# Performance work log

Measured on AMD Instinct MI355X. Metric: run time of the kernel, lower is better.

The kernel has to match this reference:

```python
import jax, jax.numpy as jnp
import numpy as np

N = 50000      # nodes
E = 1_600_000  # edges (avg degree 32)
IN = 256
HID = 64
H = 4          # heads
OUT = 128
NEG = 0.2      # LeakyReLU negative slope


def setup_inputs() -> dict:
    key = jax.random.key(0)
    ks = jax.random.split(key, 16)
    def p(i, shape):
        return jax.random.normal(ks[i], shape, jnp.float32) * 0.05
    x = jax.random.normal(ks[0], (N, IN), jnp.float32)
    edge_index = jax.random.randint(ks[1], (2, E), 0, N, dtype=jnp.int64)
    return dict(
        x=x, edge_index=edge_index,
        W0=p(2, (IN, H * HID)), as0=p(3, (H, HID)), ad0=p(4, (H, HID)), b0=p(5, (H * HID,)),
        W1=p(6, (H * HID, H * HID)), as1=p(7, (H, HID)), ad1=p(8, (H, HID)), b1=p(9, (H * HID,)),
        W2=p(10, (H * HID, OUT)), as2=p(11, (1, OUT)), ad2=p(12, (1, OUT)), b2=p(13, (OUT,)),
        Wl=p(14, (H * HID, OUT)), bl=p(15, (OUT,)),
    )


def gat_conv(x, src, dst, W, a_s, a_d, b, heads, ch):
    # Linear projection -> per-head features [N, H, C]
    h = (x @ W).reshape(-1, heads, ch)
    # Per-node attention logits [N, H]
    al_s = jnp.einsum('nhc,hc->nh', h, a_s)
    al_d = jnp.einsum('nhc,hc->nh', h, a_d)
    # Per-edge logits: gather + LeakyReLU  [E2, H]
    e = jax.nn.leaky_relu(al_s[src] + al_d[dst], NEG)
    # Segment softmax over destination neighborhoods (stable)
    m = jax.ops.segment_max(e, dst, num_segments=N)
    e = jnp.exp(e - m[dst])
    s = jax.ops.segment_sum(e, dst, num_segments=N)
    a = e / s[dst]
    # Weighted scatter-add aggregation [N, H, C]
    out = jax.ops.segment_sum(a[:, :, None] * h[src], dst, num_segments=N)
    return out.reshape(N, heads * ch) + b


def reference(x, edge_index, W0, as0, ad0, b0, W1, as1, ad1, b1, W2, as2, ad2, b2, Wl, bl):
    # add self-loops (PyG GATConv default)
    loop = jnp.arange(N, dtype=edge_index.dtype)
    src = jnp.concatenate([edge_index[0], loop])
    dst = jnp.concatenate([edge_index[1], loop])
    # layer 0: in -> hid*heads (no residual at layer 0)
    h0 = gat_conv(x, src, dst, W0, as0, ad0, b0, H, HID)
    # layer 1: hid*heads -> hid*heads, residual
    h1 = gat_conv(h0, src, dst, W1, as1, ad1, b1, H, HID) + h0
    # layer 2 (last): hid*heads -> out with 1 head, residual via last_linear
    h2 = gat_conv(h1, src, dst, W2, as2, ad2, b2, 1, OUT) + (h1 @ Wl + bl)
    return h2
```

## Files before the change

kernel.cpp:

```cpp
#include <hip/hip_runtime.h>
#include <hip/hip_bf16.h>

#define N_NODES 50000
#define N_EDGES 1600000
#define E2 (N_EDGES + N_NODES)
#define NB 782
#define BCAP 3072
#define CHUNK 8192
#define NBLK_E 202

typedef __attribute__((ext_vector_type(8))) short bf16x8;
typedef __attribute__((ext_vector_type(4))) float f32x4;

static __device__ __forceinline__ float lrelu(float x) { return x > 0.f ? x : 0.2f * x; }

static __device__ __forceinline__ float b2f(ushort u) {
    union { unsigned int u; float f; } v;
    v.u = ((unsigned int)u) << 16;
    return v.f;
}
static __device__ __forceinline__ float hi2f(unsigned int u) {
    union { unsigned int u; float f; } v;
    v.u = u & 0xffff0000u;
    return v.f;
}
static __device__ __forceinline__ float lo2f(unsigned int u) {
    union { unsigned int u; float f; } v;
    v.u = u << 16;
    return v.f;
}
static __device__ __forceinline__ ushort f2b(float f) {
    union { float f; unsigned int u; } v;
    v.f = f;
    unsigned int r = v.u + 0x7FFFu + ((v.u >> 16) & 1u);
    return (ushort)(r >> 16);
}


__global__ __launch_bounds__(256) void k_bhist(const int* __restrict__ edst, int* __restrict__ hist) {
    __shared__ int cnt[NB];
    int t = threadIdx.x;
    for (int i = t; i < NB; i += 256) cnt[i] = 0;
    __syncthreads();
    int e0 = blockIdx.x * CHUNK;
    int eend = min(e0 + CHUNK, E2);
    for (int e = e0 + t; e < eend; e += 256) {
        int d = (e < N_EDGES) ? edst[e] : (e - N_EDGES);
        atomicAdd(&cnt[d >> 6], 1);
    }
    __syncthreads();
    for (int i = t; i < NB; i += 256) hist[blockIdx.x * NB + i] = cnt[i];
}

__global__ __launch_bounds__(1024) void k_colscan(const int* __restrict__ hist,
                                                  int* __restrict__ start, int* __restrict__ btotal) {
    int b = threadIdx.x;
    if (b >= NB) return;
    int run = 0;
#pragma unroll 4
    for (int blk = 0; blk < NBLK_E; ++blk) {
        int v = hist[blk * NB + b];
        start[blk * NB + b] = run;
        run += v;
    }
    btotal[b] = run;
}

__global__ __launch_bounds__(256) void k_bscan(const int* __restrict__ btotal, int* __restrict__ bbase,
                                               int* __restrict__ rowptr) {
    __shared__ int s[256];
    int t = threadIdx.x;
    int v[4];
    int sum = 0;
#pragma unroll
    for (int k = 0; k < 4; ++k) {
        int i = t * 4 + k;
        v[k] = (i < NB) ? btotal[i] : 0;
        sum += v[k];
    }
    s[t] = sum;
    __syncthreads();
    for (int off = 1; off < 256; off <<= 1) {
        int add = (t >= off) ? s[t - off] : 0;
        __syncthreads();
        s[t] += add;
        __syncthreads();
    }
    int base = s[t] - sum;
#pragma unroll
    for (int k = 0; k < 4; ++k) {
        int i = t * 4 + k;
        if (i < NB) bbase[i] = base;
        base += v[k];
    }
    if (t == 0) rowptr[N_NODES] = E2;
}

__global__ __launch_bounds__(256) void k_bscatter(const int* __restrict__ esrc, const int* __restrict__ edst,
                                                  const int* __restrict__ start, const int* __restrict__ bbase,
                                                  unsigned int* __restrict__ bbuf) {
    __shared__ int cnt[NB];
    __shared__ int cur[NB];
    __shared__ int gofs[NB];
    __shared__ int s_scan[256];
    __shared__ unsigned int s_e[CHUNK];
    int t = threadIdx.x;
    for (int i = t; i < NB; i += 256) cnt[i] = 0;
    __syncthreads();
    int e0 = blockIdx.x * CHUNK;
    int eend = min(e0 + CHUNK, E2);
    for (int e = e0 + t; e < eend; e += 256) {
        int d = (e < N_EDGES) ? edst[e] : (e - N_EDGES);
        atomicAdd(&cnt[d >> 6], 1);
    }
    __syncthreads();
    int v[4];
    int sum = 0;
#pragma unroll
    for (int k = 0; k < 4; ++k) {
        int i = t * 4 + k;
        v[k] = (i < NB) ? cnt[i] : 0;
        sum += v[k];
    }
    s_scan[t] = sum;
    __syncthreads();
    for (int off = 1; off < 256; off <<= 1) {
        int add = (t >= off) ? s_scan[t - off] : 0;
        __syncthreads();
        s_scan[t] += add;
        __syncthreads();
    }
    int run = s_scan[t] - sum;
#pragma unroll
    for (int k = 0; k < 4; ++k) {
        int i = t * 4 + k;
        if (i < NB) {
            cur[i] = run;
            gofs[i] = bbase[i] + start[blockIdx.x * NB + i] - run;
        }
        run += v[k];
    }
    __syncthreads();
    for (int e = e0 + t; e < eend; e += 256) {
        int s, d;
        if (e < N_EDGES) { s = esrc[e]; d = edst[e]; } else { s = d = e - N_EDGES; }
        int b = d >> 6;
        int pos = atomicAdd(&cur[b], 1);
        s_e[pos] = (unsigned int)s | ((unsigned int)(d & 63) << 16) | ((unsigned int)b << 22);
    }
    __syncthreads();
    int cntall = eend - e0;
    for (int i = t; i < cntall; i += 256) {
        unsigned int p = s_e[i];
        int b = p >> 22;
        bbuf[gofs[b] + i] = p & 0x3FFFFFu;
    }
}

__global__ __launch_bounds__(256) void k_build(const int* __restrict__ btotal, const int* __restrict__ bbase,
                                               const unsigned int* __restrict__ bbuf,
                                               int* __restrict__ rowptr, int* __restrict__ col) {
    const int b = blockIdx.x;
    const int t = threadIdx.x;
    const int cnt = btotal[b];
    const int base = bbase[b];
    const int node0 = b << 6;

    __shared__ unsigned int s_e[BCAP];
    __shared__ int s_deg[64];
    __shared__ int s_cur[64];

    if (t < 64) s_deg[t] = 0;
    __syncthreads();
    for (int i = t; i < cnt; i += 256) {
        unsigned int p = bbuf[(size_t)base + i];
        s_e[i] = p;
        atomicAdd(&s_deg[(p >> 16) & 63], 1);
    }
    __syncthreads();
    if (t < 64) {
        int d = s_deg[t];
        int incl = d;
#pragma unroll
        for (int off = 1; off < 64; off <<= 1) {
            int o = __shfl_up(incl, off);
            if (t >= off) incl += o;
        }
        int startl = incl - d;
        s_cur[t] = startl;
        int node = node0 + t;
        if (node < N_NODES) rowptr[node] = base + startl;
    }
    __syncthreads();
    for (int i = t; i < cnt; i += 256) {
        unsigned int p = s_e[i];
        int pos = atomicAdd(&s_cur[(p >> 16) & 63], 1);
        col[base + pos] = (int)(p & 0xFFFFu);
    }
}


__global__ void k_quant(const float* __restrict__ x, ushort* __restrict__ xb, int n4) {
    int i = blockIdx.x * 256 + threadIdx.x;
    if (i >= n4) return;
    float4 v = ((const float4*)x)[i];
    ushort4 o;
    o.x = f2b(v.x); o.y = f2b(v.y); o.z = f2b(v.z); o.w = f2b(v.w);
    ((ushort4*)xb)[i] = o;
}

__global__ void k_wt(const float* __restrict__ W, ushort* __restrict__ Wt) {
    int i = blockIdx.x * 256 + threadIdx.x;
    int k = i >> 8, n = i & 255;
    Wt[n * 256 + k] = f2b(W[i]);
}

__global__ void k_wtc(const float* __restrict__ W2, const float* __restrict__ Wl, ushort* __restrict__ Wt) {
    int i = blockIdx.x * 256 + threadIdx.x;
    int k = i >> 8, n = i & 255;
    float v = (n < 128) ? W2[k * 128 + n] : Wl[k * 128 + (n - 128)];
    Wt[n * 256 + k] = f2b(v);
}


template <bool FUSE>
__global__ __launch_bounds__(256) void k_mfma(const ushort* __restrict__ A, const ushort* __restrict__ Bt,
                                              ushort* __restrict__ Cb, int M,
                                              const float* __restrict__ a_s, const float* __restrict__ a_d,
                                              float* __restrict__ als, float* __restrict__ ald) {
    const int t = threadIdx.x;
    const int w = t >> 6, l = t & 63;
    const int lr = l & 15, lk = l >> 4;
    const int m0 = blockIdx.x * 32;
    const int n0 = w * 64;
    f32x4 acc[2][4] = {};

    int r0 = m0 + lr;      if (r0 >= M) r0 = M - 1;
    int r1 = m0 + 16 + lr; if (r1 >= M) r1 = M - 1;
    const ushort* a0p = A + (size_t)r0 * 256 + lk * 8;
    const ushort* a1p = A + (size_t)r1 * 256 + lk * 8;
    const ushort* bp  = Bt + (size_t)(n0 + lr) * 256 + lk * 8;

#pragma unroll
    for (int k0 = 0; k0 < 256; k0 += 32) {
        bf16x8 a0 = *(const bf16x8*)(a0p + k0);
        bf16x8 a1 = *(const bf16x8*)(a1p + k0);
#pragma unroll
        for (int n = 0; n < 4; ++n) {
            bf16x8 b = *(const bf16x8*)(bp + n * 16 * 256 + k0);
            acc[0][n] = __builtin_amdgcn_mfma_f32_16x16x32_bf16(a0, b, acc[0][n], 0, 0, 0);
            acc[1][n] = __builtin_amdgcn_mfma_f32_16x16x32_bf16(a1, b, acc[1][n], 0, 0, 0);
        }
    }

#pragma unroll
    for (int m = 0; m < 2; ++m) {
#pragma unroll
        for (int r = 0; r < 4; ++r) {
            int row = m0 + m * 16 + lk * 4 + r;
            if (row >= M) continue;
#pragma unroll
            for (int n = 0; n < 4; ++n) {
                Cb[(size_t)row * 256 + n0 + n * 16 + lr] = f2b(acc[m][n][r]);
            }
        }
    }

    if constexpr (FUSE) {
        float asc[4], adc[4];
#pragma unroll
        for (int n = 0; n < 4; ++n) {
            int c = n0 + n * 16 + lr;
            asc[n] = a_s[c];
            adc[n] = a_d[c];
        }
#pragma unroll
        for (int m = 0; m < 2; ++m) {
#pragma unroll
            for (int r = 0; r < 4; ++r) {
                float pa = 0.f, pd = 0.f;
#pragma unroll
                for (int n = 0; n < 4; ++n) {
                    pa += acc[m][n][r] * asc[n];
                    pd += acc[m][n][r] * adc[n];
                }
#pragma unroll
                for (int off = 1; off < 16; off <<= 1) {
                    pa += __shfl_xor(pa, off);
                    pd += __shfl_xor(pd, off);
                }
                if (lr == 0) {
                    int row = m0 + m * 16 + lk * 4 + r;
                    if (row < M) {
                        als[row * 4 + w] = pa;
                        ald[row * 4 + w] = pd;
                    }
                }
            }
        }
    }
}


template <int HEADS, int CHAN>
__global__ __launch_bounds__(256) void k_al(const ushort* __restrict__ Pb,
                                            const float* __restrict__ a_s, const float* __restrict__ a_d,
                                            float* __restrict__ als, float* __restrict__ ald) {
    int n = blockIdx.x * 4 + (threadIdx.x >> 6);
    if (n >= N_NODES) return;
    int l = threadIdx.x & 63;
    const ushort* row = Pb + (size_t)n * 256;
#pragma unroll
    for (int h = 0; h < HEADS; ++h) {
        float ps = 0.f, pd = 0.f;
#pragma unroll
        for (int c = l; c < CHAN; c += 64) {
            float v = b2f(row[h * CHAN + c]);
            ps += v * a_s[h * CHAN + c];
            pd += v * a_d[h * CHAN + c];
        }
#pragma unroll
        for (int off = 32; off > 0; off >>= 1) {
            ps += __shfl_xor(ps, off);
            pd += __shfl_xor(pd, off);
        }
        if (l == 0) { als[n * HEADS + h] = ps; ald[n * HEADS + h] = pd; }
    }
}


template <int HEADS>
__device__ __forceinline__ void load_als(const float* __restrict__ als, int src, float* v) {
    if constexpr (HEADS == 4) {
        float4 a = *(const float4*)(als + (size_t)src * 4);
        v[0] = a.x; v[1] = a.y; v[2] = a.z; v[3] = a.w;
    } else {
        v[0] = als[src];
    }
}


template <int HEADS, int CHAN, bool RESB, bool LIN, bool WRITEF, bool WRITEB>
__global__ __launch_bounds__(256) void k_aggw(
    const ushort* __restrict__ Pb,
    const float* __restrict__ als, const float* __restrict__ ald,
    const int* __restrict__ rowptr, const int* __restrict__ col,
    const float* __restrict__ bias, const float* __restrict__ bias2,
    const ushort* __restrict__ residb, float* __restrict__ out, ushort* __restrict__ outb) {
    constexpr int BLK = HEADS * CHAN;
    constexpr int CPL = BLK / 64;
    const int t = threadIdx.x;
    const int w = t >> 6, l = t & 63;
    const int n = blockIdx.x * 4 + w;
    const int rs = rowptr[n];
    const int deg = rowptr[n + 1] - rs;

    __shared__ int s_src[4][64];
    __shared__ float s_w[4][64 * HEADS];

    float aldn[HEADS];
    load_als<HEADS>(ald, n, aldn);

    float acc[CPL];
#pragma unroll
    for (int c = 0; c < CPL; ++c) acc[c] = 0.f;
    float sw[HEADS];
#pragma unroll
    for (int h = 0; h < HEADS; ++h) sw[h] = 0.f;

    const int hsel = l >> 4;

    for (int base = 0; base < deg; base += 64) {
        int j = base + l;
        if (j < deg) {
            int src = col[rs + j];
            s_src[w][l] = src;
            float av[HEADS];
            load_als<HEADS>(als, src, av);
#pragma unroll
            for (int h = 0; h < HEADS; ++h) {
                float wv = __expf(lrelu(av[h] + aldn[h]));
                s_w[w][l * HEADS + h] = wv;
                sw[h] += wv;
            }
        }
        int cnt = min(64, deg - base);
        int jj = 0;
        for (; jj + 2 <= cnt; jj += 2) {
            int s0 = __builtin_amdgcn_readfirstlane(s_src[w][jj]);
            int s1 = __builtin_amdgcn_readfirstlane(s_src[w][jj + 1]);
            if constexpr (CPL == 4) {
                float w0 = s_w[w][jj * HEADS + hsel];
                float w1 = s_w[w][(jj + 1) * HEADS + hsel];
                uint2 v0 = *(const uint2*)(Pb + (size_t)s0 * 256 + l * 4);
                uint2 v1 = *(const uint2*)(Pb + (size_t)s1 * 256 + l * 4);
                acc[0] += w0 * lo2f(v0.x); acc[1] += w0 * hi2f(v0.x);
                acc[2] += w0 * lo2f(v0.y); acc[3] += w0 * hi2f(v0.y);
                acc[0] += w1 * lo2f(v1.x); acc[1] += w1 * hi2f(v1.x);
                acc[2] += w1 * lo2f(v1.y); acc[3] += w1 * hi2f(v1.y);
            } else {
                float w0 = s_w[w][jj];
                float w1 = s_w[w][jj + 1];
                unsigned int v0 = *(const unsigned int*)(Pb + (size_t)s0 * 256 + l * 2);
                unsigned int v1 = *(const unsigned int*)(Pb + (size_t)s1 * 256 + l * 2);
                acc[0] += w0 * lo2f(v0); acc[1] += w0 * hi2f(v0);
                acc[0] += w1 * lo2f(v1); acc[1] += w1 * hi2f(v1);
            }
        }
        if (jj < cnt) {
            int s0 = __builtin_amdgcn_readfirstlane(s_src[w][jj]);
            if constexpr (CPL == 4) {
                float w0 = s_w[w][jj * HEADS + hsel];
                uint2 v0 = *(const uint2*)(Pb + (size_t)s0 * 256 + l * 4);
                acc[0] += w0 * lo2f(v0.x); acc[1] += w0 * hi2f(v0.x);
                acc[2] += w0 * lo2f(v0.y); acc[3] += w0 * hi2f(v0.y);
            } else {
                float w0 = s_w[w][jj];
                unsigned int v0 = *(const unsigned int*)(Pb + (size_t)s0 * 256 + l * 2);
                acc[0] += w0 * lo2f(v0); acc[1] += w0 * hi2f(v0);
            }
        }
    }

#pragma unroll
    for (int off = 32; off > 0; off >>= 1)
#pragma unroll
        for (int h = 0; h < HEADS; ++h) sw[h] += __shfl_xor(sw[h], off);

    float stot;
    if constexpr (HEADS == 4) {
        stot = (hsel == 0) ? sw[0] : (hsel == 1) ? sw[1] : (hsel == 2) ? sw[2] : sw[3];
    } else {
        stot = sw[0];
    }
    float rinv = 1.0f / stot;

    float r[CPL];
#pragma unroll
    for (int c = 0; c < CPL; ++c) r[c] = acc[c] * rinv + bias[l * CPL + c];
    if constexpr (RESB) {
        ushort4 rv = *(const ushort4*)(residb + (size_t)n * 256 + l * 4);
        r[0] += b2f(rv.x); r[1] += b2f(rv.y); r[2] += b2f(rv.z); r[3] += b2f(rv.w);
    }
    if constexpr (LIN) {
        unsigned int lv = *(const unsigned int*)(Pb + (size_t)n * 256 + 128 + l * 2);
        float2 bv = *(const float2*)(bias2 + l * 2);
        r[0] += lo2f(lv) + bv.x;
        r[1] += hi2f(lv) + bv.y;
    }
    if constexpr (WRITEF) {
        if constexpr (CPL == 4) {
            *(float4*)&out[(size_t)n * BLK + l * 4] = make_float4(r[0], r[1], r[2], r[3]);
        } else {
            *(float2*)&out[(size_t)n * BLK + l * 2] = make_float2(r[0], r[1]);
        }
    }
    if constexpr (WRITEB) {
        ushort4 o;
        o.x = f2b(r[0]); o.y = f2b(r[1]); o.z = f2b(r[2]); o.w = f2b(r[3]);
        *(ushort4*)&outb[(size_t)n * BLK + l * 4] = o;
    }
}


extern "C" void kernel_launch(void* const* d_in, const int* in_sizes, int n_in,
                              void* d_out, int out_size, void* d_ws, size_t ws_size,
                              hipStream_t stream) {
    const float* x   = (const float*)d_in[0];
    const int* ei    = (const int*)d_in[1];
    const int* esrc  = ei;
    const int* edst  = ei + N_EDGES;
    const float* W0  = (const float*)d_in[2];
    const float* as0 = (const float*)d_in[3];
    const float* ad0 = (const float*)d_in[4];
    const float* b0  = (const float*)d_in[5];
    const float* W1  = (const float*)d_in[6];
    const float* as1 = (const float*)d_in[7];
    const float* ad1 = (const float*)d_in[8];
    const float* b1  = (const float*)d_in[9];
    const float* W2  = (const float*)d_in[10];
    const float* as2 = (const float*)d_in[11];
    const float* ad2 = (const float*)d_in[12];
    const float* b2  = (const float*)d_in[13];
    const float* Wl  = (const float*)d_in[14];
    const float* bl  = (const float*)d_in[15];
    float* out = (float*)d_out;

    char* w = (char*)d_ws;
    auto alloc = [&](size_t bytes) { char* p = w; w += (bytes + 255) & ~(size_t)255; return p; };
    ushort* xb  = (ushort*)alloc((size_t)N_NODES * 256 * 2);
    ushort* Pb  = (ushort*)alloc((size_t)N_NODES * 256 * 2);
    ushort* h0b = (ushort*)alloc((size_t)N_NODES * 256 * 2);
    float* als = (float*)alloc((size_t)N_NODES * 4 * 4);
    float* ald = (float*)alloc((size_t)N_NODES * 4 * 4);
    ushort* Wt0 = (ushort*)alloc(256 * 256 * 2);
    ushort* Wt1 = (ushort*)alloc(256 * 256 * 2);
    ushort* Wtc = (ushort*)alloc(256 * 256 * 2);
    unsigned int* bbuf = (unsigned int*)alloc((size_t)E2 * 4);
    int* hist   = (int*)alloc((size_t)NBLK_E * NB * 4);
    int* start  = (int*)alloc((size_t)NBLK_E * NB * 4);
    int* btotal = (int*)alloc((size_t)NB * 4);
    int* bbase  = (int*)alloc((size_t)NB * 4);
    int* rowptr = (int*)alloc((size_t)(N_NODES + 1) * 4);
    int* colb   = (int*)alloc((size_t)E2 * 4);
    ushort* h1b = xb;

    k_bhist<<<NBLK_E, 256, 0, stream>>>(edst, hist);
    k_colscan<<<1, 1024, 0, stream>>>(hist, start, btotal);
    k_bscan<<<1, 256, 0, stream>>>(btotal, bbase, rowptr);
    k_bscatter<<<NBLK_E, 256, 0, stream>>>(esrc, edst, start, bbase, bbuf);
    k_build<<<NB, 256, 0, stream>>>(btotal, bbase, bbuf, rowptr, colb);

    k_quant<<<(N_NODES * 256 / 4 + 255) / 256, 256, 0, stream>>>(x, xb, N_NODES * 256 / 4);
    k_wt<<<256, 256, 0, stream>>>(W0, Wt0);
    k_wt<<<256, 256, 0, stream>>>(W1, Wt1);
    k_wtc<<<256, 256, 0, stream>>>(W2, Wl, Wtc);

    const int gm = (N_NODES + 31) / 32;
    const int ga = (N_NODES + 3) / 4;
    const int gn = N_NODES / 4;

    k_mfma<true><<<gm, 256, 0, stream>>>(xb, Wt0, Pb, N_NODES, as0, ad0, als, ald);
    k_aggw<4, 64, false, false, false, true><<<gn, 256, 0, stream>>>(
        Pb, als, ald, rowptr, colb, b0, nullptr, nullptr, nullptr, h0b);
    k_mfma<true><<<gm, 256, 0, stream>>>(h0b, Wt1, Pb, N_NODES, as1, ad1, als, ald);
    k_aggw<4, 64, true, false, false, true><<<gn, 256, 0, stream>>>(
        Pb, als, ald, rowptr, colb, b1, nullptr, h0b, nullptr, h1b);
    k_mfma<false><<<gm, 256, 0, stream>>>(h1b, Wtc, Pb, N_NODES, nullptr, nullptr, nullptr, nullptr);
    k_al<1, 128><<<ga, 256, 0, stream>>>(Pb, as2, ad2, als, ald);
    k_aggw<1, 128, false, true, true, false><<<gn, 256, 0, stream>>>(
        Pb, als, ald, rowptr, colb, b2, bl, nullptr, out, nullptr);
}
```

Measured before the change: 651.9 us.

## Bucket neighbors by source slab and sweep slabs across waves for cache locality

The CSR build now sorts each node's neighbor list by source-node slab (src>>13) and stores eight row pointers per node instead of one. The aggregation kernel gives each wave seven destination nodes spaced a grid-stride apart. All waves sweep the source slabs in the same order, so the feature gathers from Pb at any moment fall mostly in one slab of about 4 MB, which should stay cache resident. Attention weights are now computed per edge with wave-uniform scalar loads rather than batched across lanes through shared memory. The cost is serial per-edge latency chains and fewer waves overall, with more rowptr traffic.

```diff
diff --git a/kernel.cpp b/kernel.cpp
--- a/kernel.cpp
+++ b/kernel.cpp
@@ -8,6 +8,10 @@
 #define BCAP 3072
 #define CHUNK 8192
 #define NBLK_E 202
+#define NS 7
+#define RP2W 8
+#define WPG 8192
+#define NPW 7
 
 typedef __attribute__((ext_vector_type(8))) short bf16x8;
 typedef __attribute__((ext_vector_type(4))) float f32x4;
@@ -66,8 +70,7 @@
     btotal[b] = run;
 }
 
-__global__ __launch_bounds__(256) void k_bscan(const int* __restrict__ btotal, int* __restrict__ bbase,
-                                               int* __restrict__ rowptr) {
+__global__ __launch_bounds__(256) void k_bscan(const int* __restrict__ btotal, int* __restrict__ bbase) {
     __shared__ int s[256];
     int t = threadIdx.x;
     int v[4];
@@ -93,7 +96,6 @@
         if (i < NB) bbase[i] = base;
         base += v[k];
     }
-    if (t == 0) rowptr[N_NODES] = E2;
 }
 
 __global__ __launch_bounds__(256) void k_bscatter(const int* __restrict__ esrc, const int* __restrict__ edst,
@@ -159,7 +161,7 @@
 
 __global__ __launch_bounds__(256) void k_build(const int* __restrict__ btotal, const int* __restrict__ bbase,
                                                const unsigned int* __restrict__ bbuf,
-                                               int* __restrict__ rowptr, int* __restrict__ col) {
+                                               int* __restrict__ rowptr2, int* __restrict__ col) {
     const int b = blockIdx.x;
     const int t = threadIdx.x;
     const int cnt = btotal[b];
@@ -167,34 +169,45 @@
     const int node0 = b << 6;
 
     __shared__ unsigned int s_e[BCAP];
-    __shared__ int s_deg[64];
-    __shared__ int s_cur[64];
-
-    if (t < 64) s_deg[t] = 0;
+    __shared__ int s_cnt[512];
+    __shared__ int s_cur[512];
+    __shared__ int s_scan[256];
+
+    s_cnt[t] = 0; s_cnt[t + 256] = 0;
     __syncthreads();
     for (int i = t; i < cnt; i += 256) {
         unsigned int p = bbuf[(size_t)base + i];
         s_e[i] = p;
-        atomicAdd(&s_deg[(p >> 16) & 63], 1);
-    }
-    __syncthreads();
-    if (t < 64) {
-        int d = s_deg[t];
-        int incl = d;
-#pragma unroll
-        for (int off = 1; off < 64; off <<= 1) {
-            int o = __shfl_up(incl, off);
-            if (t >= off) incl += o;
-        }
-        int startl = incl - d;
-        s_cur[t] = startl;
-        int node = node0 + t;
-        if (node < N_NODES) rowptr[node] = base + startl;
+        int key = (int)((p >> 16) & 63) * 8 + (int)((p & 0xFFFFu) >> 13);
+        atomicAdd(&s_cnt[key], 1);
+    }
+    __syncthreads();
+    int v0 = s_cnt[t * 2], v1 = s_cnt[t * 2 + 1];
+    int sum = v0 + v1;
+    s_scan[t] = sum;
+    __syncthreads();
+    for (int off = 1; off < 256; off <<= 1) {
+        int add = (t >= off) ? s_scan[t - off] : 0;
+        __syncthreads();
+        s_scan[t] += add;
+        __syncthreads();
+    }
+    int run = s_scan[t] - sum;
+    s_cur[t * 2] = run;
+    s_cur[t * 2 + 1] = run + v0;
+    __syncthreads();
+    {
+        int key0 = t * 2, key1 = t * 2 + 1;
+        int n0 = node0 + (key0 >> 3);
+        int n1 = node0 + (key1 >> 3);
+        if (n0 < N_NODES) rowptr2[(size_t)n0 * RP2W + (key0 & 7)] = base + s_cur[key0];
+        if (n1 < N_NODES) rowptr2[(size_t)n1 * RP2W + (key1 & 7)] = base + s_cur[key1];
     }
     __syncthreads();
     for (int i = t; i < cnt; i += 256) {
         unsigned int p = s_e[i];
-        int pos = atomicAdd(&s_cur[(p >> 16) & 63], 1);
+        int key = (int)((p >> 16) & 63) * 8 + (int)((p & 0xFFFFu) >> 13);
+        int pos = atomicAdd(&s_cur[key], 1);
         col[base + pos] = (int)(p & 0xFFFFu);
     }
 }
@@ -329,136 +342,104 @@
 }
 
 
-template <int HEADS>
-__device__ __forceinline__ void load_als(const float* __restrict__ als, int src, float* v) {
-    if constexpr (HEADS == 4) {
-        float4 a = *(const float4*)(als + (size_t)src * 4);
-        v[0] = a.x; v[1] = a.y; v[2] = a.z; v[3] = a.w;
-    } else {
-        v[0] = als[src];
-    }
-}
-
-
-template <int HEADS, int CHAN, bool RESB, bool LIN, bool WRITEF, bool WRITEB>
-__global__ __launch_bounds__(256) void k_aggw(
+template <int HEADS, int CPL, bool RESB, bool LIN, bool WRITEF, bool WRITEB>
+__global__ __launch_bounds__(256) void k_aggp(
     const ushort* __restrict__ Pb,
     const float* __restrict__ als, const float* __restrict__ ald,
-    const int* __restrict__ rowptr, const int* __restrict__ col,
+    const int* __restrict__ rowptr2, const int* __restrict__ col,
     const float* __restrict__ bias, const float* __restrict__ bias2,
     const ushort* __restrict__ residb, float* __restrict__ out, ushort* __restrict__ outb) {
-    constexpr int BLK = HEADS * CHAN;
-    constexpr int CPL = BLK / 64;
+    constexpr int BLK = 64 * CPL;
     const int t = threadIdx.x;
     const int w = t >> 6, l = t & 63;
-    const int n = blockIdx.x * 4 + w;
-    const int rs = rowptr[n];
-    const int deg = rowptr[n + 1] - rs;
-
-    __shared__ int s_src[4][64];
-    __shared__ float s_w[4][64 * HEADS];
-
-    float aldn[HEADS];
-    load_als<HEADS>(ald, n, aldn);
-
-    float acc[CPL];
-#pragma unroll
-    for (int c = 0; c < CPL; ++c) acc[c] = 0.f;
-    float sw[HEADS];
-#pragma unroll
-    for (int h = 0; h < HEADS; ++h) sw[h] = 0.f;
-
-    const int hsel = l >> 4;
-
-    for (int base = 0; base < deg; base += 64) {
-        int j = base + l;
-        if (j < deg) {
-            int src = col[rs + j];
-            s_src[w][l] = src;
-            float av[HEADS];
-            load_als<HEADS>(als, src, av);
-#pragma unroll
-            for (int h = 0; h < HEADS; ++h) {
-                float wv = __expf(lrelu(av[h] + aldn[h]));
-                s_w[w][l * HEADS + h] = wv;
-                sw[h] += wv;
+    const int wid = blockIdx.x * 4 + w;
+    const int hsel = (HEADS == 4) ? (l >> 4) : 0;
+
+    float acc[NPW][CPL];
+    float sw[NPW];
+    float aldk[NPW];
+#pragma unroll
+    for (int k = 0; k < NPW; ++k) {
+        sw[k] = 0.f;
+#pragma unroll
+        for (int c = 0; c < CPL; ++c) acc[k][c] = 0.f;
+        int n = wid + k * WPG;
+        aldk[k] = (n < N_NODES) ? ald[(size_t)n * HEADS + hsel] : 0.f;
+    }
+
+    for (int s = 0; s < NS; ++s) {
+#pragma unroll
+        for (int k = 0; k < NPW; ++k) {
+            int n = wid + k * WPG;
+            if (n >= N_NODES) continue;
+            int e  = __builtin_amdgcn_readfirstlane(rowptr2[(size_t)n * RP2W + s]);
+            int ee = __builtin_amdgcn_readfirstlane(rowptr2[(size_t)n * RP2W + s + 1]);
+            for (; e + 2 <= ee; e += 2) {
+                int s0 = __builtin_amdgcn_readfirstlane(col[e]);
+                int s1 = __builtin_amdgcn_readfirstlane(col[e + 1]);
+                float w0 = __expf(lrelu(als[(size_t)s0 * HEADS + hsel] + aldk[k]));
+                float w1 = __expf(lrelu(als[(size_t)s1 * HEADS + hsel] + aldk[k]));
+                if constexpr (CPL == 4) {
+                    uint2 v0 = *(const uint2*)(Pb + (size_t)s0 * 256 + l * 4);
+                    uint2 v1 = *(const uint2*)(Pb + (size_t)s1 * 256 + l * 4);
+                    acc[k][0] += w0 * lo2f(v0.x); acc[k][1] += w0 * hi2f(v0.x);
+                    acc[k][2] += w0 * lo2f(v0.y); acc[k][3] += w0 * hi2f(v0.y);
+                    acc[k][0] += w1 * lo2f(v1.x); acc[k][1] += w1 * hi2f(v1.x);
+                    acc[k][2] += w1 * lo2f(v1.y); acc[k][3] += w1 * hi2f(v1.y);
+                } else {
+                    unsigned int v0 = *(const unsigned int*)(Pb + (size_t)s0 * 256 + l * 2);
+                    unsigned int v1 = *(const unsigned int*)(Pb + (size_t)s1 * 256 + l * 2);
+                    acc[k][0] += w0 * lo2f(v0); acc[k][1] += w0 * hi2f(v0);
+                    acc[k][0] += w1 * lo2f(v1); acc[k][1] += w1 * hi2f(v1);
+                }
+                sw[k] += w0 + w1;
             }
-        }
-        int cnt = min(64, deg - base);
-        int jj = 0;
-        for (; jj + 2 <= cnt; jj += 2) {
-            int s0 = __builtin_amdgcn_readfirstlane(s_src[w][jj]);
-            int s1 = __builtin_amdgcn_readfirstlane(s_src[w][jj + 1]);
+            if (e < ee) {
+                int s0 = __builtin_amdgcn_readfirstlane(col[e]);
+                float w0 = __expf(lrelu(als[(size_t)s0 * HEADS + hsel] + aldk[k]));
+                if constexpr (CPL == 4) {
+                    uint2 v0 = *(const uint2*)(Pb + (size_t)s0 * 256 + l * 4);
+                    acc[k][0] += w0 * lo2f(v0.x); acc[k][1] += w0 * hi2f(v0.x);
+                    acc[k][2] += w0 * lo2f(v0.y); acc[k][3] += w0 * hi2f(v0.y);
+                } else {
+                    unsigned int v0 = *(const unsigned int*)(Pb + (size_t)s0 * 256 + l * 2);
+                    acc[k][0] += w0 * lo2f(v0); acc[k][1] += w0 * hi2f(v0);
+                }
+                sw[k] += w0;
+            }
+        }
+    }
+
+#pragma unroll
+    for (int k = 0; k < NPW; ++k) {
+        int n = wid + k * WPG;
+        if (n >= N_NODES) continue;
+        float rinv = 1.0f / sw[k];
+        float r[CPL];
+#pragma unroll
+        for (int c = 0; c < CPL; ++c) r[c] = acc[k][c] * rinv + bias[l * CPL + c];
+        if constexpr (RESB) {
+            ushort4 rv = *(const ushort4*)(residb + (size_t)n * 256 + l * 4);
+            r[0] += b2f(rv.x); r[1] += b2f(rv.y); r[2] += b2f(rv.z); r[3] += b2f(rv.w);
+        }
+        if constexpr (LIN) {
+            unsigned int lv = *(const unsigned int*)(Pb + (size_t)n * 256 + 128 + l * 2);
+            float2 bv = *(const float2*)(bias2 + l * 2);
+            r[0] += lo2f(lv) + bv.x;
+            r[1] += hi2f(lv) + bv.y;
+        }
+        if constexpr (WRITEF) {
             if constexpr (CPL == 4) {
-                float w0 = s_w[w][jj * HEADS + hsel];
-                float w1 = s_w[w][(jj + 1) * HEADS + hsel];
-                uint2 v0 = *(const uint2*)(Pb + (size_t)s0 * 256 + l * 4);
-                uint2 v1 = *(const uint2*)(Pb + (size_t)s1 * 256 + l * 4);
-                acc[0] += w0 * lo2f(v0.x); acc[1] += w0 * hi2f(v0.x);
-                acc[2] += w0 * lo2f(v0.y); acc[3] += w0 * hi2f(v0.y);
-                acc[0] += w1 * lo2f(v1.x); acc[1] += w1 * hi2f(v1.x);
-                acc[2] += w1 * lo2f(v1.y); acc[3] += w1 * hi2f(v1.y);
+                *(float4*)&out[(size_t)n * BLK + l * 4] = make_float4(r[0], r[1], r[2], r[3]);
             } else {
-                float w0 = s_w[w][jj];
-                float w1 = s_w[w][jj + 1];
-                unsigned int v0 = *(const unsigned int*)(Pb + (size_t)s0 * 256 + l * 2);
-                unsigned int v1 = *(const unsigned int*)(Pb + (size_t)s1 * 256 + l * 2);
-                acc[0] += w0 * lo2f(v0); acc[1] += w0 * hi2f(v0);
-                acc[0] += w1 * lo2f(v1); acc[1] += w1 * hi2f(v1);
+                *(float2*)&out[(size_t)n * BLK + l * 2] = make_float2(r[0], r[1]);
             }
         }
-        if (jj < cnt) {
-            int s0 = __builtin_amdgcn_readfirstlane(s_src[w][jj]);
-            if constexpr (CPL == 4) {
-                float w0 = s_w[w][jj * HEADS + hsel];
-                uint2 v0 = *(const uint2*)(Pb + (size_t)s0 * 256 + l * 4);
-                acc[0] += w0 * lo2f(v0.x); acc[1] += w0 * hi2f(v0.x);
-                acc[2] += w0 * lo2f(v0.y); acc[3] += w0 * hi2f(v0.y);
-            } else {
-                float w0 = s_w[w][jj];
-                unsigned int v0 = *(const unsigned int*)(Pb + (size_t)s0 * 256 + l * 2);
-                acc[0] += w0 * lo2f(v0); acc[1] += w0 * hi2f(v0);
-            }
-        }
-    }
-
-#pragma unroll
-    for (int off = 32; off > 0; off >>= 1)
-#pragma unroll
-        for (int h = 0; h < HEADS; ++h) sw[h] += __shfl_xor(sw[h], off);
-
-    float stot;
-    if constexpr (HEADS == 4) {
-        stot = (hsel == 0) ? sw[0] : (hsel == 1) ? sw[1] : (hsel == 2) ? sw[2] : sw[3];
-    } else {
-        stot = sw[0];
-    }
-    float rinv = 1.0f / stot;
-
-    float r[CPL];
-#pragma unroll
-    for (int c = 0; c < CPL; ++c) r[c] = acc[c] * rinv + bias[l * CPL + c];
-    if constexpr (RESB) {
-        ushort4 rv = *(const ushort4*)(residb + (size_t)n * 256 + l * 4);
-        r[0] += b2f(rv.x); r[1] += b2f(rv.y); r[2] += b2f(rv.z); r[3] += b2f(rv.w);
-    }
-    if constexpr (LIN) {
-        unsigned int lv = *(const unsigned int*)(Pb + (size_t)n * 256 + 128 + l * 2);
-        float2 bv = *(const float2*)(bias2 + l * 2);
-        r[0] += lo2f(lv) + bv.x;
-        r[1] += hi2f(lv) + bv.y;
-    }
-    if constexpr (WRITEF) {
-        if constexpr (CPL == 4) {
-            *(float4*)&out[(size_t)n * BLK + l * 4] = make_float4(r[0], r[1], r[2], r[3]);
-        } else {
-            *(float2*)&out[(size_t)n * BLK + l * 2] = make_float2(r[0], r[1]);
-        }
-    }
-    if constexpr (WRITEB) {
-        ushort4 o;
-        o.x = f2b(r[0]); o.y = f2b(r[1]); o.z = f2b(r[2]); o.w = f2b(r[3]);
-        *(ushort4*)&outb[(size_t)n * BLK + l * 4] = o;
+        if constexpr (WRITEB) {
+            ushort4 o;
+            o.x = f2b(r[0]); o.y = f2b(r[1]); o.z = f2b(r[2]); o.w = f2b(r[3]);
+            *(ushort4*)&outb[(size_t)n * BLK + l * 4] = o;
+        }
     }
 }
 
@@ -501,15 +482,15 @@
     int* start  = (int*)alloc((size_t)NBLK_E * NB * 4);
     int* btotal = (int*)alloc((size_t)NB * 4);
     int* bbase  = (int*)alloc((size_t)NB * 4);
-    int* rowptr = (int*)alloc((size_t)(N_NODES + 1) * 4);
+    int* rowptr2 = (int*)alloc((size_t)N_NODES * RP2W * 4);
     int* colb   = (int*)alloc((size_t)E2 * 4);
     ushort* h1b = xb;
 
     k_bhist<<<NBLK_E, 256, 0, stream>>>(edst, hist);
     k_colscan<<<1, 1024, 0, stream>>>(hist, start, btotal);
-    k_bscan<<<1, 256, 0, stream>>>(btotal, bbase, rowptr);
+    k_bscan<<<1, 256, 0, stream>>>(btotal, bbase);
     k_bscatter<<<NBLK_E, 256, 0, stream>>>(esrc, edst, start, bbase, bbuf);
-    k_build<<<NB, 256, 0, stream>>>(btotal, bbase, bbuf, rowptr, colb);
+    k_build<<<NB, 256, 0, stream>>>(btotal, bbase, bbuf, rowptr2, colb);
 
     k_quant<<<(N_NODES * 256 / 4 + 255) / 256, 256, 0, stream>>>(x, xb, N_NODES * 256 / 4);
     k_wt<<<256, 256, 0, stream>>>(W0, Wt0);
@@ -518,16 +499,16 @@
 
     const int gm = (N_NODES + 31) / 32;
     const int ga = (N_NODES + 3) / 4;
-    const int gn = N_NODES / 4;
+    const int gp = WPG / 4;
 
     k_mfma<true><<<gm, 256, 0, stream>>>(xb, Wt0, Pb, N_NODES, as0, ad0, als, ald);
-    k_aggw<4, 64, false, false, false, true><<<gn, 256, 0, stream>>>(
-        Pb, als, ald, rowptr, colb, b0, nullptr, nullptr, nullptr, h0b);
+    k_aggp<4, 4, false, false, false, true><<<gp, 256, 0, stream>>>(
+        Pb, als, ald, rowptr2, colb, b0, nullptr, nullptr, nullptr, h0b);
     k_mfma<true><<<gm, 256, 0, stream>>>(h0b, Wt1, Pb, N_NODES, as1, ad1, als, ald);
-    k_aggw<4, 64, true, false, false, true><<<gn, 256, 0, stream>>>(
-        Pb, als, ald, rowptr, colb, b1, nullptr, h0b, nullptr, h1b);
+    k_aggp<4, 4, true, false, false, true><<<gp, 256, 0, stream>>>(
+        Pb, als, ald, rowptr2, colb, b1, nullptr, h0b, nullptr, h1b);
     k_mfma<false><<<gm, 256, 0, stream>>>(h1b, Wtc, Pb, N_NODES, nullptr, nullptr, nullptr, nullptr);
     k_al<1, 128><<<ga, 256, 0, stream>>>(Pb, as2, ad2, als, ald);
-    k_aggw<1, 128, false, true, true, false><<<gn, 256, 0, stream>>>(
-        Pb, als, ald, rowptr, colb, b2, bl, nullptr, out, nullptr);
-}
+    k_aggp<1, 2, false, true, true, false><<<gp, 256, 0, stream>>>(
+        Pb, als, ald, rowptr2, colb, b2, bl, nullptr, out, nullptr);
+}
```

New measurement: 739.3 us. +13.4%, slower.
